# Kernel tuning notes

Measured on AMD Instinct MI355X. Metric: run time of the kernel, lower is better.

Reference implementation:

```python
import jax, jax.numpy as jnp
import numpy as np

B, L, D, H, NL, V, W = 4, 2048, 512, 8, 4, 258, 8
HD = D // H


def setup_inputs() -> dict:
    key = jax.random.key(0)
    ks = jax.random.split(key, 12)
    s = 0.02
    x = jax.random.randint(ks[0], (B, L), 0, V, dtype=jnp.int32)
    patch_lengths = jnp.full((B, 256), W, dtype=jnp.int32)  # sum over patches == L
    emb = jax.random.normal(ks[1], (V, D), jnp.float32) * s
    ent_w = jax.random.normal(ks[2], (D, 1), jnp.float32) * s
    ent_b = jnp.zeros((D,), jnp.float32)
    qkv_w = jax.random.normal(ks[3], (NL, 3 * D, D), jnp.float32) * s
    qkv_b = jnp.zeros((NL, 3 * D), jnp.float32)
    ao_w = jax.random.normal(ks[4], (NL, D, D), jnp.float32) * s
    ao_b = jnp.zeros((NL, D), jnp.float32)
    ln1_s = jnp.ones((NL, D), jnp.float32)
    ln1_b = jnp.zeros((NL, D), jnp.float32)
    ln2_s = jnp.ones((NL, D), jnp.float32)
    ln2_b = jnp.zeros((NL, D), jnp.float32)
    ff1_w = jax.random.normal(ks[5], (NL, 4 * D, D), jnp.float32) * s
    ff1_b = jnp.zeros((NL, 4 * D), jnp.float32)
    ff2_w = jax.random.normal(ks[6], (NL, D, 4 * D), jnp.float32) * s
    ff2_b = jnp.zeros((NL, D), jnp.float32)
    out_w = jax.random.normal(ks[7], (V, D), jnp.float32) * s
    return {"emb": emb, "ent_w": ent_w, "ent_b": ent_b, "qkv_w": qkv_w,
            "qkv_b": qkv_b, "ao_w": ao_w, "ao_b": ao_b, "ln1_s": ln1_s,
            "ln1_b": ln1_b, "ln2_s": ln2_s, "ln2_b": ln2_b, "ff1_w": ff1_w,
            "ff1_b": ff1_b, "ff2_w": ff2_w, "ff2_b": ff2_b, "out_w": out_w,
            "x": x, "patch_lengths": patch_lengths}


def _layernorm(h, scale, bias, eps=1e-5):
    mu = jnp.mean(h, axis=-1, keepdims=True)
    var = jnp.mean(jnp.square(h - mu), axis=-1, keepdims=True)
    return (h - mu) * jax.lax.rsqrt(var + eps) * scale + bias


def _entropy_features(x, dtype):
    # fused sliding-window histogram via one-hot cumsum (replaces per-window bincount loop)
    onehot = jax.nn.one_hot(x, 256, dtype=dtype)            # [B, L, 256]
    c = jnp.cumsum(onehot, axis=1)
    cpad = jnp.concatenate([jnp.zeros_like(c[:, :1]), c], axis=1)
    counts = cpad[:, W:] - cpad[:, :-W]                     # [B, L-W+1, 256]
    p = counts / W
    ent = -jnp.sum(p * jnp.log2(p + 1e-10), axis=-1)        # zero-count terms contribute exactly 0
    full = jnp.zeros(x.shape, dtype).at[:, :x.shape[1] - W + 1].set(ent)
    return full[..., None]                                  # [B, L, 1]


def _block(h, p):
    qkv_w, qkv_b, ao_w, ao_b, l1s, l1b, l2s, l2b, f1w, f1b, f2w, f2b = p
    g = _layernorm(h, l1s, l1b)
    qkv = g @ qkv_w.T + qkv_b                                # [B, L, 3D]
    q, k, v = jnp.split(qkv, 3, axis=-1)
    q = q.reshape(B, L, H, HD)
    k = k.reshape(B, L, H, HD)
    v = v.reshape(B, L, H, HD)
    scores = jnp.einsum('blhd,bmhd->bhlm', q, k) / np.sqrt(HD).astype(h.dtype)
    attn = jax.nn.softmax(scores, axis=-1)
    o = jnp.einsum('bhlm,bmhd->blhd', attn, v).reshape(B, L, D)
    h = h + o @ ao_w.T + ao_b
    g = _layernorm(h, l2s, l2b)
    g = jax.nn.gelu(g @ f1w.T + f1b, approximate=False) @ f2w.T + f2b
    return h + g, None


def reference(emb, ent_w, ent_b, qkv_w, qkv_b, ao_w, ao_b, ln1_s, ln1_b,
              ln2_s, ln2_b, ff1_w, ff1_b, ff2_w, ff2_b, out_w, x, patch_lengths):
    tok = emb[x]                                             # [B, L, D]
    ent = _entropy_features(x, tok.dtype)                    # [B, L, 1]
    ent_emb = ent * ent_w[:, 0] + ent_b                      # Linear(1, D)
    h = tok + ent_emb
    h, _ = jax.lax.scan(_block, h,
                        (qkv_w, qkv_b, ao_w, ao_b, ln1_s, ln1_b,
                         ln2_s, ln2_b, ff1_w, ff1_b, ff2_w, ff2_b))
    # NOTE: the original module's global_transformer/patch-pool branch does not
    # feed the returned logits (dead code); logits come from the local stream h.
    logits = h @ out_w.T                                     # [B, L, V]
    return logits
```

## Files before the change

kernel.cpp:

```cpp
#include <hip/hip_runtime.h>
#include <hip/hip_bf16.h>
#include <math.h>

#define BB 4
#define LL 2048
#define DD 512
#define HH 8
#define NLAYER 4
#define VV 258
#define WW 8
#define HDIM 64
#define MM (BB * LL)
#define VPAD 384

#define C8 0.18033688f

typedef __attribute__((ext_vector_type(8))) short short8v;
typedef __attribute__((ext_vector_type(4))) float float4v;

typedef __attribute__((address_space(3))) unsigned int lds_u32;
typedef const __attribute__((address_space(1))) unsigned int glb_u32;

__device__ __forceinline__ unsigned short f2bf(float x) {
    unsigned int u = __float_as_uint(x);
    unsigned int r = (u + 0x7fffu + ((u >> 16) & 1u)) >> 16;
    return (unsigned short)r;
}

__device__ __forceinline__ unsigned lds_addr(const void* p) {
    return (unsigned)(size_t)(__attribute__((address_space(3))) const void*)p;
}

#define E0 (NLAYER * 3 * DD * DD)
#define E1 (E0 + NLAYER * DD * DD)
#define E2 (E1 + NLAYER * 4 * DD * DD)
#define E3 (E2 + NLAYER * 4 * DD * DD)
#define E4 (E3 + VPAD * DD)

__global__ __launch_bounds__(256)
void cvt_all_kernel(const float* __restrict__ qkv_w, const float* __restrict__ ao_w,
                    const float* __restrict__ ff1_w, const float* __restrict__ ff2_w,
                    const float* __restrict__ out_w, unsigned short* __restrict__ dst)
{
    int i = (blockIdx.x * 256 + threadIdx.x) * 4;
    float4 v;
    if (i < E0)      v = *reinterpret_cast<const float4*>(qkv_w + i);
    else if (i < E1) v = *reinterpret_cast<const float4*>(ao_w + (i - E0));
    else if (i < E2) v = *reinterpret_cast<const float4*>(ff1_w + (i - E1));
    else if (i < E3) v = *reinterpret_cast<const float4*>(ff2_w + (i - E2));
    else {
        int idx = i - E3;
        if ((idx >> 9) < VV) v = *reinterpret_cast<const float4*>(out_w + idx);
        else                 v = (float4){0.f, 0.f, 0.f, 0.f};
    }
    uint2 pk;
    pk.x = (unsigned)f2bf(v.x) | ((unsigned)f2bf(v.y) << 16);
    pk.y = (unsigned)f2bf(v.z) | ((unsigned)f2bf(v.w) << 16);
    *reinterpret_cast<uint2*>(dst + i) = pk;
}

__global__ __launch_bounds__(256)
void embed_ln_kernel(const int* __restrict__ x,
                     const float* __restrict__ emb,
                     const float* __restrict__ ent_w,
                     const float* __restrict__ ent_b,
                     const float* __restrict__ ln_s,
                     const float* __restrict__ ln_b,
                     float* __restrict__ h,
                     unsigned short* __restrict__ g)
{
    int w = threadIdx.x >> 6, lane = threadIdx.x & 63;
    int row = blockIdx.x * 4 + w;
    int b = row / LL, l = row % LL;

    float ent = 0.f;
    if (l <= LL - WW) {
        int win[WW];
        #pragma unroll
        for (int i = 0; i < WW; i++) win[i] = x[b * LL + l + i];
        float s = 0.f;
        #pragma unroll
        for (int i = 0; i < WW; i++) {
            if (win[i] < 256) {
                int c = 0;
                #pragma unroll
                for (int j = 0; j < WW; j++) c += (win[j] == win[i]) ? 1 : 0;
                s += log2f((float)c * 0.125f + 1e-10f);
            }
        }
        ent = -s * 0.125f;
    }

    int tok = x[row];
    const float* erow = emb + (size_t)tok * DD + lane * 8;
    float v[8], ew[8], eb[8];
    *reinterpret_cast<float4*>(v)      = *reinterpret_cast<const float4*>(erow);
    *reinterpret_cast<float4*>(v + 4)  = *reinterpret_cast<const float4*>(erow + 4);
    *reinterpret_cast<float4*>(ew)     = *reinterpret_cast<const float4*>(ent_w + lane * 8);
    *reinterpret_cast<float4*>(ew + 4) = *reinterpret_cast<const float4*>(ent_w + lane * 8 + 4);
    *reinterpret_cast<float4*>(eb)     = *reinterpret_cast<const float4*>(ent_b + lane * 8);
    *reinterpret_cast<float4*>(eb + 4) = *reinterpret_cast<const float4*>(ent_b + lane * 8 + 4);

    float sum = 0.f, sq = 0.f;
    #pragma unroll
    for (int i = 0; i < 8; i++) {
        v[i] = v[i] + ent * ew[i] + eb[i];
        sum += v[i]; sq += v[i] * v[i];
    }
    float* hr = h + (size_t)row * DD + lane * 8;
    *reinterpret_cast<float4*>(hr)     = *reinterpret_cast<const float4*>(v);
    *reinterpret_cast<float4*>(hr + 4) = *reinterpret_cast<const float4*>(v + 4);

    #pragma unroll
    for (int off = 32; off > 0; off >>= 1) {
        sum += __shfl_xor(sum, off);
        sq  += __shfl_xor(sq, off);
    }
    float mu = sum * (1.f / DD);
    float var = sq * (1.f / DD) - mu * mu;
    float rstd = rsqrtf(var + 1e-5f);

    float s8[8], bi[8];
    *reinterpret_cast<float4*>(s8)     = *reinterpret_cast<const float4*>(ln_s + lane * 8);
    *reinterpret_cast<float4*>(s8 + 4) = *reinterpret_cast<const float4*>(ln_s + lane * 8 + 4);
    *reinterpret_cast<float4*>(bi)     = *reinterpret_cast<const float4*>(ln_b + lane * 8);
    *reinterpret_cast<float4*>(bi + 4) = *reinterpret_cast<const float4*>(ln_b + lane * 8 + 4);

    unsigned int pk[4];
    #pragma unroll
    for (int i = 0; i < 4; i++) {
        unsigned short lo = f2bf((v[2*i]   - mu) * rstd * s8[2*i]   + bi[2*i]);
        unsigned short hi = f2bf((v[2*i+1] - mu) * rstd * s8[2*i+1] + bi[2*i+1]);
        pk[i] = (unsigned)lo | ((unsigned)hi << 16);
    }
    *reinterpret_cast<uint4*>(g + (size_t)row * DD + lane * 8) =
        *reinterpret_cast<const uint4*>(pk);
}

__global__ __launch_bounds__(256)
void ln_kernel(const float* __restrict__ h,
               const float* __restrict__ scale,
               const float* __restrict__ bias,
               unsigned short* __restrict__ g)
{
    int w = threadIdx.x >> 6, lane = threadIdx.x & 63;
    int row = blockIdx.x * 4 + w;
    const float* hr = h + (size_t)row * DD + lane * 8;

    float v[8];
    *reinterpret_cast<float4*>(v)     = *reinterpret_cast<const float4*>(hr);
    *reinterpret_cast<float4*>(v + 4) = *reinterpret_cast<const float4*>(hr + 4);

    float sum = 0.f, sq = 0.f;
    #pragma unroll
    for (int i = 0; i < 8; i++) { sum += v[i]; sq += v[i] * v[i]; }
    #pragma unroll
    for (int off = 32; off > 0; off >>= 1) {
        sum += __shfl_xor(sum, off);
        sq  += __shfl_xor(sq, off);
    }
    float mu = sum * (1.f / DD);
    float var = sq * (1.f / DD) - mu * mu;
    float rstd = rsqrtf(var + 1e-5f);

    float s[8], bi[8];
    *reinterpret_cast<float4*>(s)      = *reinterpret_cast<const float4*>(scale + lane * 8);
    *reinterpret_cast<float4*>(s + 4)  = *reinterpret_cast<const float4*>(scale + lane * 8 + 4);
    *reinterpret_cast<float4*>(bi)     = *reinterpret_cast<const float4*>(bias + lane * 8);
    *reinterpret_cast<float4*>(bi + 4) = *reinterpret_cast<const float4*>(bias + lane * 8 + 4);

    unsigned int pk[4];
    #pragma unroll
    for (int i = 0; i < 4; i++) {
        unsigned short lo = f2bf((v[2*i]   - mu) * rstd * s[2*i]   + bi[2*i]);
        unsigned short hi = f2bf((v[2*i+1] - mu) * rstd * s[2*i+1] + bi[2*i+1]);
        pk[i] = (unsigned)lo | ((unsigned)hi << 16);
    }
    *reinterpret_cast<uint4*>(g + (size_t)row * DD + lane * 8) =
        *reinterpret_cast<const uint4*>(pk);
}

template<bool HAS_BIAS, bool GELU, bool RESID, int OMODE>
__global__ __launch_bounds__(256)
void gemm_mfma(const unsigned short* __restrict__ A,
               const unsigned short* __restrict__ W,
               const float* __restrict__ bias,
               const float* __restrict__ resid,
               void* __restrict__ Cv,
               unsigned short* __restrict__ Cb,
               int Nn, int Kk)
{
    __shared__ unsigned short As[2][128 * 64];
    __shared__ unsigned short Bs[2][128 * 64];

    int t = threadIdx.x;
    int w = t >> 6, lane = t & 63;
    int wr = w >> 1, wc = w & 1;
    int l15 = lane & 15, l4 = lane >> 4;
    int m0 = blockIdx.y * 128, n0 = blockIdx.x * 128;

    int lrow = lane >> 3;
    int segp = (lane & 7) ^ lrow;

    float4v acc[4][4];
    #pragma unroll
    for (int i = 0; i < 4; i++)
        #pragma unroll
        for (int j = 0; j < 4; j++)
            acc[i][j] = (float4v){0.f, 0.f, 0.f, 0.f};

    #define STAGE(buf, k0) do {                                                   \
        _Pragma("unroll")                                                         \
        for (int i_ = 0; i_ < 4; i_++) {                                          \
            int r_ = i_ * 32 + w * 8 + lrow;                                      \
            __builtin_amdgcn_global_load_lds(                                     \
                (glb_u32*)(A + (size_t)(m0 + r_) * Kk + (k0) + segp * 8),         \
                (lds_u32*)(As[buf] + i_ * 2048 + w * 512), 16, 0, 0);             \
            __builtin_amdgcn_global_load_lds(                                     \
                (glb_u32*)(W + (size_t)(n0 + r_) * Kk + (k0) + segp * 8),         \
                (lds_u32*)(Bs[buf] + i_ * 2048 + w * 512), 16, 0, 0);             \
        } } while (0)

    int nk = Kk >> 6;
    STAGE(0, 0);
    for (int kt = 0; kt < nk; kt++) {
        int cur = kt & 1;
        if (kt + 1 < nk) {
            STAGE(cur ^ 1, (kt + 1) << 6);
            __builtin_amdgcn_sched_barrier(0);
            asm volatile("s_waitcnt vmcnt(8)");
            __builtin_amdgcn_sched_barrier(0);
        } else {
            __builtin_amdgcn_sched_barrier(0);
            asm volatile("s_waitcnt vmcnt(0)");
            __builtin_amdgcn_sched_barrier(0);
        }
        __builtin_amdgcn_s_barrier();

        const char* asb = (const char*)As[cur];
        const char* bsb = (const char*)Bs[cur];
        #pragma unroll
        for (int kc = 0; kc < 2; kc++) {
            short8v af[4], bfr[4];
            #pragma unroll
            for (int mf = 0; mf < 4; mf++) {
                int row = wr * 64 + mf * 16 + l15;
                int off = (row * 128 + kc * 64 + l4 * 16) ^ ((row & 7) << 4);
                af[mf] = *reinterpret_cast<const short8v*>(asb + off);
            }
            #pragma unroll
            for (int nf = 0; nf < 4; nf++) {
                int row = wc * 64 + nf * 16 + l15;
                int off = (row * 128 + kc * 64 + l4 * 16) ^ ((row & 7) << 4);
                bfr[nf] = *reinterpret_cast<const short8v*>(bsb + off);
            }
            #pragma unroll
            for (int mf = 0; mf < 4; mf++)
                #pragma unroll
                for (int nf = 0; nf < 4; nf++)
                    acc[mf][nf] = __builtin_amdgcn_mfma_f32_16x16x32_bf16(
                        af[mf], bfr[nf], acc[mf][nf], 0, 0, 0);
        }
        __builtin_amdgcn_s_barrier();
    }
    #undef STAGE

    #pragma unroll
    for (int mf = 0; mf < 4; mf++)
        #pragma unroll
        for (int nf = 0; nf < 4; nf++)
            #pragma unroll
            for (int r = 0; r < 4; r++) {
                int m = m0 + wr * 64 + mf * 16 + l4 * 4 + r;
                int n = n0 + wc * 64 + nf * 16 + l15;
                if (n < Nn) {
                    float v = acc[mf][nf][r];
                    if (HAS_BIAS) v += bias[n];
                    if (GELU)     v = 0.5f * v * (1.f + erff(v * 0.70710678118654752f));
                    if (RESID)    v += resid[(size_t)m * Nn + n];
                    if (OMODE == 1) {
                        ((unsigned short*)Cv)[(size_t)m * Nn + n] = f2bf(v);
                    } else {
                        ((float*)Cv)[(size_t)m * Nn + n] = v;
                        if (OMODE == 2) Cb[(size_t)m * Nn + n] = f2bf(v);
                    }
                }
            }
}

__global__ __launch_bounds__(512, 2)
void attn_mfma(const unsigned short* __restrict__ qkv, unsigned short* __restrict__ o)
{
    __shared__ unsigned short Kl[2][64 * 64];
    __shared__ unsigned short Vs[2][64 * 64];
    __shared__ unsigned short Pl[8 * 16 * 64];
    __shared__ float Scl[8][16];

    int t = threadIdx.x, w = t >> 6, lane = t & 63;
    int l15 = lane & 15, l4 = lane >> 4;

    int flat = blockIdx.x;
    int swz = (flat & 7) * 64 + (flat >> 3);
    int qt = swz & 15, hh = (swz >> 4) & 7, b = swz >> 7;

    int q0 = qt * 128 + w * 16;
    const int RS = 3 * DD;

    short8v qf[2];
    #pragma unroll
    for (int dh = 0; dh < 2; dh++) {
        size_t addr = (size_t)(b * LL + q0 + l15) * RS + hh * HDIM + dh * 32 + l4 * 8;
        qf[dh] = *reinterpret_cast<const short8v*>(qkv + addr);
    }

    float4v o_acc[4];
    #pragma unroll
    for (int dt = 0; dt < 4; dt++) o_acc[dt] = (float4v){0.f, 0.f, 0.f, 0.f};
    float l_run = 0.f;

    char* pbase = (char*)Pl + w * 2048;

    int lrow8 = lane >> 3;
    int ksegp = (lane & 7) ^ lrow8;
    int vrow = ((t >> 5) << 2) | ((t >> 1) & 3);
    int vseg = (((t >> 3) & 3) << 1) | (t & 1);
    const unsigned short* kgl = qkv + (size_t)(b * LL + w * 8 + lrow8) * RS
                              + hh * HDIM + DD + ksegp * 8;
    const unsigned short* vgl = qkv + (size_t)(b * LL + vrow) * RS
                              + hh * HDIM + 2 * DD + vseg * 8;
    const int step = 64 * RS;

    #define ASTAGE(buf) do {                                                      \
        __builtin_amdgcn_global_load_lds((glb_u32*)kgl,                           \
            (lds_u32*)(Kl[buf] + w * 512), 16, 0, 0);                             \
        __builtin_amdgcn_global_load_lds((glb_u32*)vgl,                           \
            (lds_u32*)(Vs[buf] + w * 512), 16, 0, 0);                             \
        kgl += step; vgl += step; } while (0)

    unsigned vtrbase = lds_addr(Vs) + ((lane >> 4) << 10)
                     + (((lane >> 2) & 3) << 5) + ((lane & 3) << 3);
    unsigned pswz = (unsigned)((l15 & 7) << 4);
    unsigned pa0 = lds_addr(pbase) + ((unsigned)(l15 * 128 + l4 * 16) ^ pswz);
    unsigned pa1 = lds_addr(pbase) + ((unsigned)(l15 * 128 + 64 + l4 * 16) ^ pswz);

    ASTAGE(0);
    asm volatile("s_waitcnt vmcnt(0)");
    __syncthreads();

    for (int kb = 0; kb < LL / 64; kb++) {
        int cur = kb & 1;
        if (kb + 1 < LL / 64) ASTAGE(cur ^ 1);

        const char* klc = (const char*)Kl[cur];
        unsigned vb = vtrbase + cur * 8192;

        float4v s_acc[4];
        __builtin_amdgcn_s_setprio(1);
        #pragma unroll
        for (int nt = 0; nt < 4; nt++) {
            s_acc[nt] = (float4v){0.f, 0.f, 0.f, 0.f};
            #pragma unroll
            for (int dh = 0; dh < 2; dh++) {
                int row = nt * 16 + l15;
                int off = (row * 128 + dh * 64 + l4 * 16) ^ ((row & 7) << 4);
                short8v kf = *reinterpret_cast<const short8v*>(klc + off);
                s_acc[nt] = __builtin_amdgcn_mfma_f32_16x16x32_bf16(kf, qf[dh], s_acc[nt], 0, 0, 0);
            }
        }
        __builtin_amdgcn_s_setprio(0);

        float ps = 0.f;
        #pragma unroll
        for (int nt = 0; nt < 4; nt++) {
            float p0 = __builtin_amdgcn_exp2f(s_acc[nt][0] * C8);
            float p1 = __builtin_amdgcn_exp2f(s_acc[nt][1] * C8);
            float p2 = __builtin_amdgcn_exp2f(s_acc[nt][2] * C8);
            float p3 = __builtin_amdgcn_exp2f(s_acc[nt][3] * C8);
            ps += (p0 + p1) + (p2 + p3);
            unsigned int pk0, pk1;
            asm("v_cvt_pk_bf16_f32 %0, %1, %2" : "=v"(pk0) : "v"(p0), "v"(p1));
            asm("v_cvt_pk_bf16_f32 %0, %1, %2" : "=v"(pk1) : "v"(p2), "v"(p3));
            uint2 pk; pk.x = pk0; pk.y = pk1;
            int off = (l15 * 128 + nt * 32 + l4 * 8) ^ ((l15 & 7) << 4);
            *reinterpret_cast<uint2*>(pbase + off) = pk;
        }
        l_run += ps;

        short8v pf0, pf1;
        asm volatile("ds_read_b128 %0, %1" : "=v"(pf0) : "v"(pa0) : "memory");
        asm volatile("ds_read_b128 %0, %1" : "=v"(pf1) : "v"(pa1) : "memory");
        unsigned long long a0, a1, a2, a3, a4, a5, a6, a7;
        unsigned long long b0, b1, b2, b3, b4, b5, b6, b7;
        unsigned ab0 = vb, ab1 = vb + 4096;
        asm volatile("ds_read_b64_tr_b16 %0, %1" : "=v"(a0) : "v"(ab0));
        asm volatile("ds_read_b64_tr_b16 %0, %1" : "=v"(a1) : "v"(ab0 + 512));
        asm volatile("ds_read_b64_tr_b16 %0, %1" : "=v"(a2) : "v"(ab0 + 128));
        asm volatile("ds_read_b64_tr_b16 %0, %1" : "=v"(a3) : "v"(ab0 + 640));
        asm volatile("ds_read_b64_tr_b16 %0, %1" : "=v"(a4) : "v"(ab0 + 256));
        asm volatile("ds_read_b64_tr_b16 %0, %1" : "=v"(a5) : "v"(ab0 + 768));
        asm volatile("ds_read_b64_tr_b16 %0, %1" : "=v"(a6) : "v"(ab0 + 384));
        asm volatile("ds_read_b64_tr_b16 %0, %1" : "=v"(a7) : "v"(ab0 + 896));
        asm volatile("ds_read_b64_tr_b16 %0, %1" : "=v"(b0) : "v"(ab1));
        asm volatile("ds_read_b64_tr_b16 %0, %1" : "=v"(b1) : "v"(ab1 + 512));
        asm volatile("ds_read_b64_tr_b16 %0, %1" : "=v"(b2) : "v"(ab1 + 128));
        asm volatile("ds_read_b64_tr_b16 %0, %1" : "=v"(b3) : "v"(ab1 + 640));
        asm volatile("ds_read_b64_tr_b16 %0, %1" : "=v"(b4) : "v"(ab1 + 256));
        asm volatile("ds_read_b64_tr_b16 %0, %1" : "=v"(b5) : "v"(ab1 + 768));
        asm volatile("ds_read_b64_tr_b16 %0, %1" : "=v"(b6) : "v"(ab1 + 384));
        asm volatile("ds_read_b64_tr_b16 %0, %1" : "=v"(b7) : "v"(ab1 + 896));
        union { unsigned long long q[2]; short8v v; } u0, u1, u2, u3;
        __builtin_amdgcn_s_setprio(1);
        asm volatile("s_waitcnt lgkmcnt(12)");
        __builtin_amdgcn_sched_barrier(0);
        u0.q[0] = a0; u0.q[1] = a1;
        u1.q[0] = a2; u1.q[1] = a3;
        o_acc[0] = __builtin_amdgcn_mfma_f32_16x16x32_bf16(pf0, u0.v, o_acc[0], 0, 0, 0);
        o_acc[1] = __builtin_amdgcn_mfma_f32_16x16x32_bf16(pf0, u1.v, o_acc[1], 0, 0, 0);
        asm volatile("s_waitcnt lgkmcnt(8)");
        __builtin_amdgcn_sched_barrier(0);
        u2.q[0] = a4; u2.q[1] = a5;
        u3.q[0] = a6; u3.q[1] = a7;
        o_acc[2] = __builtin_amdgcn_mfma_f32_16x16x32_bf16(pf0, u2.v, o_acc[2], 0, 0, 0);
        o_acc[3] = __builtin_amdgcn_mfma_f32_16x16x32_bf16(pf0, u3.v, o_acc[3], 0, 0, 0);
        asm volatile("s_waitcnt lgkmcnt(4)");
        __builtin_amdgcn_sched_barrier(0);
        u0.q[0] = b0; u0.q[1] = b1;
        u1.q[0] = b2; u1.q[1] = b3;
        o_acc[0] = __builtin_amdgcn_mfma_f32_16x16x32_bf16(pf1, u0.v, o_acc[0], 0, 0, 0);
        o_acc[1] = __builtin_amdgcn_mfma_f32_16x16x32_bf16(pf1, u1.v, o_acc[1], 0, 0, 0);
        asm volatile("s_waitcnt lgkmcnt(0)");
        __builtin_amdgcn_sched_barrier(0);
        u2.q[0] = b4; u2.q[1] = b5;
        u3.q[0] = b6; u3.q[1] = b7;
        o_acc[2] = __builtin_amdgcn_mfma_f32_16x16x32_bf16(pf1, u2.v, o_acc[2], 0, 0, 0);
        o_acc[3] = __builtin_amdgcn_mfma_f32_16x16x32_bf16(pf1, u3.v, o_acc[3], 0, 0, 0);
        __builtin_amdgcn_s_setprio(0);

        asm volatile("s_waitcnt vmcnt(0)");
        __syncthreads();
    }
    #undef ASTAGE

    float lt = l_run;
    lt += __shfl_xor(lt, 16);
    lt += __shfl_xor(lt, 32);
    if (l4 == 0) Scl[w][l15] = 1.f / lt;
    float4 iv = *reinterpret_cast<const float4*>(&Scl[w][l4 * 4]);
    float invs[4] = {iv.x, iv.y, iv.z, iv.w};
    #pragma unroll
    for (int r = 0; r < 4; r++) {
        int qg = q0 + l4 * 4 + r;
        #pragma unroll
        for (int dt = 0; dt < 4; dt++) {
            o[(size_t)(b * LL + qg) * DD + hh * HDIM + dt * 16 + l15] =
                f2bf(o_acc[dt][r] * invs[r]);
        }
    }
}

extern "C" void kernel_launch(void* const* d_in, const int* in_sizes, int n_in,
                              void* d_out, int out_size, void* d_ws, size_t ws_size,
                              hipStream_t stream)
{
    const float* emb    = (const float*)d_in[0];
    const float* ent_w  = (const float*)d_in[1];
    const float* ent_b  = (const float*)d_in[2];
    const float* qkv_w  = (const float*)d_in[3];
    const float* qkv_b  = (const float*)d_in[4];
    const float* ao_w   = (const float*)d_in[5];
    const float* ao_b   = (const float*)d_in[6];
    const float* ln1_s  = (const float*)d_in[7];
    const float* ln1_b  = (const float*)d_in[8];
    const float* ln2_s  = (const float*)d_in[9];
    const float* ln2_b  = (const float*)d_in[10];
    const float* ff1_w  = (const float*)d_in[11];
    const float* ff1_b  = (const float*)d_in[12];
    const float* ff2_w  = (const float*)d_in[13];
    const float* ff2_b  = (const float*)d_in[14];
    const float* out_w  = (const float*)d_in[15];
    const int*   x      = (const int*)d_in[16];

    float* out = (float*)d_out;

    const int NQW = NLAYER * 3 * DD * DD;
    const int NAW = NLAYER * DD * DD;
    const int NF1 = NLAYER * 4 * DD * DD;
    const int NF2 = NLAYER * DD * 4 * DD;

    char* p = (char*)d_ws;
    unsigned short* wq  = (unsigned short*)p; p += (size_t)NQW * 2;
    unsigned short* wa  = (unsigned short*)p; p += (size_t)NAW * 2;
    unsigned short* w1  = (unsigned short*)p; p += (size_t)NF1 * 2;
    unsigned short* w2  = (unsigned short*)p; p += (size_t)NF2 * 2;
    unsigned short* wob = (unsigned short*)p; p += (size_t)VPAD * DD * 2;
    float*          h   = (float*)p;          p += (size_t)MM * DD * 4;
    unsigned short* hb  = (unsigned short*)p; p += (size_t)MM * DD * 2;
    unsigned short* gb  = (unsigned short*)p; p += (size_t)MM * DD * 2;
    unsigned short* ob  = (unsigned short*)p; p += (size_t)MM * DD * 2;
    unsigned short* bb  = (unsigned short*)p; p += (size_t)MM * 4 * DD * 2;

    dim3 blk(256);

    cvt_all_kernel<<<E4 / 1024, blk, 0, stream>>>(qkv_w, ao_w, ff1_w, ff2_w, out_w, wq);

    embed_ln_kernel<<<MM / 4, blk, 0, stream>>>(x, emb, ent_w, ent_b,
                                                ln1_s, ln1_b, h, gb);

    for (int layer = 0; layer < NLAYER; layer++) {
        const unsigned short* qw = wq + (size_t)layer * 3 * DD * DD;
        const unsigned short* aw = wa + (size_t)layer * DD * DD;
        const unsigned short* f1 = w1 + (size_t)layer * 4 * DD * DD;
        const unsigned short* f2 = w2 + (size_t)layer * DD * 4 * DD;
        const float* qb  = qkv_b + (size_t)layer * 3 * DD;
        const float* ab  = ao_b  + (size_t)layer * DD;
        const float* l1s = ln1_s + (size_t)layer * DD;
        const float* l1b = ln1_b + (size_t)layer * DD;
        const float* l2s = ln2_s + (size_t)layer * DD;
        const float* l2b = ln2_b + (size_t)layer * DD;
        const float* f1b = ff1_b + (size_t)layer * 4 * DD;
        const float* f2b = ff2_b + (size_t)layer * DD;

        if (layer > 0)
            ln_kernel<<<MM / 4, blk, 0, stream>>>(h, l1s, l1b, gb);

        {
            dim3 grid((3 * DD) / 128, MM / 128);
            gemm_mfma<true, false, false, 1><<<grid, blk, 0, stream>>>(
                gb, qw, qb, nullptr, bb, nullptr, 3 * DD, DD);
        }

        attn_mfma<<<512, 512, 0, stream>>>(bb, ob);

        {
            dim3 grid(DD / 128, MM / 128);
            gemm_mfma<true, false, true, 0><<<grid, blk, 0, stream>>>(
                ob, aw, ab, h, h, nullptr, DD, DD);
        }

        ln_kernel<<<MM / 4, blk, 0, stream>>>(h, l2s, l2b, gb);

        {
            dim3 grid((4 * DD) / 128, MM / 128);
            gemm_mfma<true, true, false, 1><<<grid, blk, 0, stream>>>(
                gb, f1, f1b, nullptr, bb, nullptr, 4 * DD, DD);
        }

        {
            dim3 grid(DD / 128, MM / 128);
            if (layer == NLAYER - 1)
                gemm_mfma<true, false, true, 2><<<grid, blk, 0, stream>>>(
                    bb, f2, f2b, h, h, hb, DD, 4 * DD);
            else
                gemm_mfma<true, false, true, 0><<<grid, blk, 0, stream>>>(
                    bb, f2, f2b, h, h, nullptr, DD, 4 * DD);
        }
    }

    {
        dim3 grid(VPAD / 128, MM / 128);
        gemm_mfma<false, false, false, 0><<<grid, blk, 0, stream>>>(
            hb, wob, nullptr, nullptr, out, nullptr, VV, DD);
    }
}
```

Measured before the change: 746.1 us.

## Store residual stream in bf16 and use 64-row tiles for narrow GEMMs

Result: no change. 747.6 us (+0.2%).

```diff
diff --git a/kernel.cpp b/kernel.cpp
--- a/kernel.cpp
+++ b/kernel.cpp
@@ -25,6 +25,9 @@
     unsigned int u = __float_as_uint(x);
     unsigned int r = (u + 0x7fffu + ((u >> 16) & 1u)) >> 16;
     return (unsigned short)r;
+}
+__device__ __forceinline__ float bf2f(unsigned short u) {
+    return __uint_as_float((unsigned)u << 16);
 }
 
 __device__ __forceinline__ unsigned lds_addr(const void* p) {
@@ -66,7 +69,7 @@
                      const float* __restrict__ ent_b,
                      const float* __restrict__ ln_s,
                      const float* __restrict__ ln_b,
-                     float* __restrict__ h,
+                     unsigned short* __restrict__ h,
                      unsigned short* __restrict__ g)
 {
     int w = threadIdx.x >> 6, lane = threadIdx.x & 63;
@@ -107,9 +110,12 @@
         v[i] = v[i] + ent * ew[i] + eb[i];
         sum += v[i]; sq += v[i] * v[i];
     }
-    float* hr = h + (size_t)row * DD + lane * 8;
-    *reinterpret_cast<float4*>(hr)     = *reinterpret_cast<const float4*>(v);
-    *reinterpret_cast<float4*>(hr + 4) = *reinterpret_cast<const float4*>(v + 4);
+    unsigned int hpk[4];
+    #pragma unroll
+    for (int i = 0; i < 4; i++)
+        hpk[i] = (unsigned)f2bf(v[2*i]) | ((unsigned)f2bf(v[2*i+1]) << 16);
+    *reinterpret_cast<uint4*>(h + (size_t)row * DD + lane * 8) =
+        *reinterpret_cast<const uint4*>(hpk);
 
     #pragma unroll
     for (int off = 32; off > 0; off >>= 1) {
@@ -138,18 +144,22 @@
 }
 
 __global__ __launch_bounds__(256)
-void ln_kernel(const float* __restrict__ h,
+void ln_kernel(const unsigned short* __restrict__ h,
                const float* __restrict__ scale,
                const float* __restrict__ bias,
                unsigned short* __restrict__ g)
 {
     int w = threadIdx.x >> 6, lane = threadIdx.x & 63;
     int row = blockIdx.x * 4 + w;
-    const float* hr = h + (size_t)row * DD + lane * 8;
-
+
+    uint4 raw = *reinterpret_cast<const uint4*>(h + (size_t)row * DD + lane * 8);
+    const unsigned* rw = reinterpret_cast<const unsigned*>(&raw);
     float v[8];
-    *reinterpret_cast<float4*>(v)     = *reinterpret_cast<const float4*>(hr);
-    *reinterpret_cast<float4*>(v + 4) = *reinterpret_cast<const float4*>(hr + 4);
+    #pragma unroll
+    for (int i = 0; i < 4; i++) {
+        v[2*i]   = __uint_as_float(rw[i] << 16);
+        v[2*i+1] = __uint_as_float(rw[i] & 0xffff0000u);
+    }
 
     float sum = 0.f, sq = 0.f;
     #pragma unroll
@@ -180,24 +190,28 @@
         *reinterpret_cast<const uint4*>(pk);
 }
 
-template<bool HAS_BIAS, bool GELU, bool RESID, int OMODE>
-__global__ __launch_bounds__(256)
+template<bool HAS_BIAS, bool GELU, bool RESID, int OMODE, int MT>
+__global__ __launch_bounds__(MT * 2)
 void gemm_mfma(const unsigned short* __restrict__ A,
                const unsigned short* __restrict__ W,
                const float* __restrict__ bias,
-               const float* __restrict__ resid,
+               const unsigned short* __restrict__ resid,
                void* __restrict__ Cv,
-               unsigned short* __restrict__ Cb,
                int Nn, int Kk)
 {
-    __shared__ unsigned short As[2][128 * 64];
+    constexpr int NW = MT / 32;
+    constexpr int BLOADS = 512 / MT;
+    constexpr int VMN = 4 + BLOADS;
+
+    __shared__ unsigned short As[2][MT * 64];
     __shared__ unsigned short Bs[2][128 * 64];
 
     int t = threadIdx.x;
     int w = t >> 6, lane = t & 63;
-    int wr = w >> 1, wc = w & 1;
+    int wr = (MT == 128) ? (w >> 1) : 0;
+    int wc = (MT == 128) ? (w & 1) : w;
     int l15 = lane & 15, l4 = lane >> 4;
-    int m0 = blockIdx.y * 128, n0 = blockIdx.x * 128;
+    int m0 = blockIdx.y * MT, n0 = blockIdx.x * 128;
 
     int lrow = lane >> 3;
     int segp = (lane & 7) ^ lrow;
@@ -212,13 +226,17 @@
     #define STAGE(buf, k0) do {                                                   \
         _Pragma("unroll")                                                         \
         for (int i_ = 0; i_ < 4; i_++) {                                          \
-            int r_ = i_ * 32 + w * 8 + lrow;                                      \
+            int r_ = i_ * (NW * 8) + w * 8 + lrow;                                \
             __builtin_amdgcn_global_load_lds(                                     \
                 (glb_u32*)(A + (size_t)(m0 + r_) * Kk + (k0) + segp * 8),         \
-                (lds_u32*)(As[buf] + i_ * 2048 + w * 512), 16, 0, 0);             \
+                (lds_u32*)(As[buf] + i_ * (NW * 512) + w * 512), 16, 0, 0);       \
+        }                                                                         \
+        _Pragma("unroll")                                                         \
+        for (int i_ = 0; i_ < BLOADS; i_++) {                                     \
+            int r_ = i_ * (NW * 8) + w * 8 + lrow;                                \
             __builtin_amdgcn_global_load_lds(                                     \
                 (glb_u32*)(W + (size_t)(n0 + r_) * Kk + (k0) + segp * 8),         \
-                (lds_u32*)(Bs[buf] + i_ * 2048 + w * 512), 16, 0, 0);             \
+                (lds_u32*)(Bs[buf] + i_ * (NW * 512) + w * 512), 16, 0, 0);       \
         } } while (0)
 
     int nk = Kk >> 6;
@@ -228,7 +246,8 @@
         if (kt + 1 < nk) {
             STAGE(cur ^ 1, (kt + 1) << 6);
             __builtin_amdgcn_sched_barrier(0);
-            asm volatile("s_waitcnt vmcnt(8)");
+            if constexpr (VMN == 8)  asm volatile("s_waitcnt vmcnt(8)");
+            else                     asm volatile("s_waitcnt vmcnt(12)");
             __builtin_amdgcn_sched_barrier(0);
         } else {
             __builtin_amdgcn_sched_barrier(0);
@@ -277,13 +296,11 @@
                     float v = acc[mf][nf][r];
                     if (HAS_BIAS) v += bias[n];
                     if (GELU)     v = 0.5f * v * (1.f + erff(v * 0.70710678118654752f));
-                    if (RESID)    v += resid[(size_t)m * Nn + n];
-                    if (OMODE == 1) {
+                    if (RESID)    v += bf2f(resid[(size_t)m * Nn + n]);
+                    if (OMODE == 1)
                         ((unsigned short*)Cv)[(size_t)m * Nn + n] = f2bf(v);
-                    } else {
+                    else
                         ((float*)Cv)[(size_t)m * Nn + n] = v;
-                        if (OMODE == 2) Cb[(size_t)m * Nn + n] = f2bf(v);
-                    }
                 }
             }
 }
@@ -493,8 +510,7 @@
     unsigned short* w1  = (unsigned short*)p; p += (size_t)NF1 * 2;
     unsigned short* w2  = (unsigned short*)p; p += (size_t)NF2 * 2;
     unsigned short* wob = (unsigned short*)p; p += (size_t)VPAD * DD * 2;
-    float*          h   = (float*)p;          p += (size_t)MM * DD * 4;
-    unsigned short* hb  = (unsigned short*)p; p += (size_t)MM * DD * 2;
+    unsigned short* h   = (unsigned short*)p; p += (size_t)MM * DD * 2;
     unsigned short* gb  = (unsigned short*)p; p += (size_t)MM * DD * 2;
     unsigned short* ob  = (unsigned short*)p; p += (size_t)MM * DD * 2;
     unsigned short* bb  = (unsigned short*)p; p += (size_t)MM * 4 * DD * 2;
@@ -525,40 +541,36 @@
 
         {
             dim3 grid((3 * DD) / 128, MM / 128);
-            gemm_mfma<true, false, false, 1><<<grid, blk, 0, stream>>>(
-                gb, qw, qb, nullptr, bb, nullptr, 3 * DD, DD);
+            gemm_mfma<true, false, false, 1, 128><<<grid, 256, 0, stream>>>(
+                gb, qw, qb, nullptr, bb, 3 * DD, DD);
         }
 
         attn_mfma<<<512, 512, 0, stream>>>(bb, ob);
 
         {
-            dim3 grid(DD / 128, MM / 128);
-            gemm_mfma<true, false, true, 0><<<grid, blk, 0, stream>>>(
-                ob, aw, ab, h, h, nullptr, DD, DD);
+            dim3 grid(DD / 128, MM / 64);
+            gemm_mfma<true, false, true, 1, 64><<<grid, 128, 0, stream>>>(
+                ob, aw, ab, h, h, DD, DD);
         }
 
         ln_kernel<<<MM / 4, blk, 0, stream>>>(h, l2s, l2b, gb);
 
         {
             dim3 grid((4 * DD) / 128, MM / 128);
-            gemm_mfma<true, true, false, 1><<<grid, blk, 0, stream>>>(
-                gb, f1, f1b, nullptr, bb, nullptr, 4 * DD, DD);
+            gemm_mfma<true, true, false, 1, 128><<<grid, 256, 0, stream>>>(
+                gb, f1, f1b, nullptr, bb, 4 * DD, DD);
         }
 
         {
-            dim3 grid(DD / 128, MM / 128);
-            if (layer == NLAYER - 1)
-                gemm_mfma<true, false, true, 2><<<grid, blk, 0, stream>>>(
-                    bb, f2, f2b, h, h, hb, DD, 4 * DD);
-            else
-                gemm_mfma<true, false, true, 0><<<grid, blk, 0, stream>>>(
-                    bb, f2, f2b, h, h, nullptr, DD, 4 * DD);
+            dim3 grid(DD / 128, MM / 64);
+            gemm_mfma<true, false, true, 1, 64><<<grid, 128, 0, stream>>>(
+                bb, f2, f2b, h, h, DD, 4 * DD);
         }
     }
 
     {
-        dim3 grid(VPAD / 128, MM / 128);
-        gemm_mfma<false, false, false, 0><<<grid, blk, 0, stream>>>(
-            hb, wob, nullptr, nullptr, out, nullptr, VV, DD);
-    }
-}
+        dim3 grid(VPAD / 128, MM / 64);
+        gemm_mfma<false, false, false, 0, 64><<<grid, 128, 0, stream>>>(
+            h, wob, nullptr, nullptr, out, VV, DD);
+    }
+}
```
